# Kernel optimization log

Hardware: AMD Instinct MI355X
Metric: run time of the kernel (lower is better)

## Reference

```python
import jax, jax.numpy as jnp
import numpy as np

B, S, V, D = 4, 2048, 50265, 768
H_LF, DH = 12, 64          # longformer-base heads
C, W = 256, 256            # chunk size, one-sided window
DFF = 3072
NH, DK = 4, 768            # outer MultiHeadAttention(n_head=4, d_k=d_v=768)


def layer_norm(x, g, b, eps=1e-5):
    mu = jnp.mean(x, axis=-1, keepdims=True)
    var = jnp.var(x, axis=-1, keepdims=True)
    return (x - mu) * jax.lax.rsqrt(var + eps) * g + b


def _overlap_chunks(t):
    # t: [B,H,S,dh] -> [B,H,nc,3c,dh] key blocks (chunks j-1,j,j+1, zero-padded at ends)
    nc = S // C
    tp = jnp.pad(t, ((0, 0), (0, 0), (C, C), (0, 0)))
    tr = tp.reshape(t.shape[0], t.shape[1], nc + 2, C, t.shape[-1])
    return jnp.concatenate([tr[:, :, :nc], tr[:, :, 1:nc + 1], tr[:, :, 2:]], axis=3)


def sliding_window_attn(q, k, v):
    # exact band attention: query i attends keys j with |i-j| <= W
    nc = S // C
    qc = q.reshape(q.shape[0], q.shape[1], nc, C, DH)
    kb = _overlap_chunks(k)
    vb = _overlap_chunks(v)
    scores = jnp.einsum('bhncd,bhnkd->bhnck', qc, kb) / np.sqrt(DH)
    ci = jnp.arange(C)[:, None]
    ki = jnp.arange(3 * C)[None, :]
    band = jnp.abs(ki - C - ci) <= W                      # [c,3c]
    n = jnp.arange(nc)[:, None]
    kpos = n * C - C + jnp.arange(3 * C)[None, :]
    valid = (kpos >= 0) & (kpos < S)                      # [nc,3c]
    mask = band[None, :, :] & valid[:, None, :]           # [nc,c,3c]
    scores = jnp.where(mask[None, None], scores, -1e9)
    a = jax.nn.softmax(scores, axis=-1)
    out = jnp.einsum('bhnck,bhnkd->bhncd', a, vb)
    return out.reshape(q.shape)


def longformer_layer(x, emb, pos, ln_e_g, ln_e_b, lf_wq, lf_wk, lf_wv, lf_wo,
                     ln1_g, ln1_b, w1, w2, ln2_g, ln2_b):
    h = layer_norm(emb[x] + pos[None], ln_e_g, ln_e_b)    # [B,S,D]
    def heads(w):
        return (h @ w).reshape(B, S, H_LF, DH).transpose(0, 2, 1, 3)
    q, k, v = heads(lf_wq), heads(lf_wk), heads(lf_wv)
    a = sliding_window_attn(q, k, v)                      # [B,H,S,dh]
    a = a.transpose(0, 2, 1, 3).reshape(B, S, D) @ lf_wo
    h = layer_norm(h + a, ln1_g, ln1_b)
    f = jax.nn.gelu(h @ w1) @ w2
    return layer_norm(h + f, ln2_g, ln2_b)


def mha_and_pool(x, out_lf, mha_wq, mha_wk, mha_wv, mha_fc, mha_ln_g, mha_ln_b):
    residual = out_lf
    def heads(w):
        return (out_lf @ w).reshape(B, S, NH, DK).transpose(0, 2, 1, 3)
    q, k, v = heads(mha_wq), heads(mha_wk), heads(mha_wv)
    scores = jnp.einsum('bhqd,bhkd->bhqk', q, k) / np.sqrt(DK)
    key_mask = (x != 0)[:, None, None, :]
    scores = jnp.where(key_mask, scores, -1e9)
    a = jax.nn.softmax(scores, axis=-1)
    o = jnp.einsum('bhqk,bhkd->bhqd', a, v)
    o = o.transpose(0, 2, 1, 3).reshape(B, S, NH * DK) @ mha_fc
    out_attn = layer_norm(o + residual, mha_ln_g, mha_ln_b)
    return jnp.max(out_attn, axis=1)                      # max_pool1d over seq -> [B,D]


def setup_inputs() -> dict:
    key = jax.random.key(0)
    ks = jax.random.split(key, 16)
    s = 0.02
    d = {
        'x': jax.random.randint(ks[0], (B, S), 0, V),
        'emb': jax.random.normal(ks[1], (V, D), jnp.float32) * s,
        'pos': jax.random.normal(ks[2], (S, D), jnp.float32) * s,
        'ln_e_g': jnp.ones((D,), jnp.float32), 'ln_e_b': jnp.zeros((D,), jnp.float32),
        'lf_wq': jax.random.normal(ks[3], (D, D), jnp.float32) * s,
        'lf_wk': jax.random.normal(ks[4], (D, D), jnp.float32) * s,
        'lf_wv': jax.random.normal(ks[5], (D, D), jnp.float32) * s,
        'lf_wo': jax.random.normal(ks[6], (D, D), jnp.float32) * s,
        'ln1_g': jnp.ones((D,), jnp.float32), 'ln1_b': jnp.zeros((D,), jnp.float32),
        'w1': jax.random.normal(ks[7], (D, DFF), jnp.float32) * s,
        'w2': jax.random.normal(ks[8], (DFF, D), jnp.float32) * s,
        'ln2_g': jnp.ones((D,), jnp.float32), 'ln2_b': jnp.zeros((D,), jnp.float32),
        'mha_wq': jax.random.normal(ks[9], (D, NH * DK), jnp.float32) * s,
        'mha_wk': jax.random.normal(ks[10], (D, NH * DK), jnp.float32) * s,
        'mha_wv': jax.random.normal(ks[11], (D, NH * DK), jnp.float32) * s,
        'mha_fc': jax.random.normal(ks[12], (NH * DK, D), jnp.float32) * s,
        'mha_ln_g': jnp.ones((D,), jnp.float32), 'mha_ln_b': jnp.zeros((D,), jnp.float32),
    }
    return d


def reference(x, emb, pos, ln_e_g, ln_e_b, lf_wq, lf_wk, lf_wv, lf_wo,
              ln1_g, ln1_b, w1, w2, ln2_g, ln2_b,
              mha_wq, mha_wk, mha_wv, mha_fc, mha_ln_g, mha_ln_b):
    out_lf = longformer_layer(x, emb, pos, ln_e_g, ln_e_b, lf_wq, lf_wk, lf_wv, lf_wo,
                              ln1_g, ln1_b, w1, w2, ln2_g, ln2_b)
    out_lf = jax.lax.stop_gradient(out_lf)  # torch.no_grad() around longformer
    return mha_and_pool(x, out_lf, mha_wq, mha_wk, mha_wv, mha_fc, mha_ln_g, mha_ln_b)
```

## Files before the change

### kernel.cpp

```cpp
#include <hip/hip_runtime.h>
#include <hip/hip_bf16.h>
#include <math.h>

#define DEV static __device__ __forceinline__

typedef unsigned short u16;
typedef __attribute__((ext_vector_type(8))) __bf16 bf16x8;
typedef __attribute__((ext_vector_type(4))) float f32x4;

constexpr int SL  = 2048;
constexpr int DM  = 768;
constexpr int CC  = 256;
constexpr int NC  = 8;
constexpr int DH  = 64;
constexpr int DFF = 3072;
constexpr int DKM = 768;

DEV float b2f(u16 u){ union{float f; unsigned u;} c; c.u = ((unsigned)u)<<16; return c.f; }
DEV u16 f2b(float f){ union{float f; unsigned u;} c; c.f=f; unsigned r=(c.u + 0x7fffu + ((c.u>>16)&1u))>>16; return (u16)r; }

DEV void gld16(u16* lds, const u16* g){
  __builtin_amdgcn_global_load_lds((const __attribute__((address_space(1))) void*)g,
                                   (__attribute__((address_space(3))) void*)lds, 16, 0, 0);
}

DEV float wred_sum(float v){
#pragma unroll
  for (int o=32;o;o>>=1) v += __shfl_xor(v,o,64);
  return v;
}
DEV float wred_max(float v){
#pragma unroll
  for (int o=32;o;o>>=1) v = fmaxf(v, __shfl_xor(v,o,64));
  return v;
}
DEV float bred_sum(float v, float* sm){
  v = wred_sum(v);
  if ((threadIdx.x & 63)==0) sm[threadIdx.x>>6] = v;
  __syncthreads();
  float r = sm[0]+sm[1]+sm[2]+sm[3];
  __syncthreads();
  return r;
}
DEV float bred_max(float v, float* sm){
  v = wred_max(v);
  if ((threadIdx.x & 63)==0) sm[threadIdx.x>>6] = v;
  __syncthreads();
  float r = fmaxf(fmaxf(sm[0],sm[1]), fmaxf(sm[2],sm[3]));
  __syncthreads();
  return r;
}

#define MFMA_PH(MH, NH) \
  { _Pragma("unroll") for (int mi2=0; mi2<4; ++mi2) { \
      _Pragma("unroll") for (int ni2=0; ni2<2; ++ni2) { \
        acc[(MH)*4+mi2][(NH)*2+ni2] = __builtin_amdgcn_mfma_f32_16x16x32_bf16(Af[mi2][0], Bf[(NH)*2+ni2][0], acc[(MH)*4+mi2][(NH)*2+ni2], 0,0,0); \
        acc[(MH)*4+mi2][(NH)*2+ni2] = __builtin_amdgcn_mfma_f32_16x16x32_bf16(Af[mi2][1], Bf[(NH)*2+ni2][1], acc[(MH)*4+mi2][(NH)*2+ni2], 0,0,0); } } }

#define PHASE_SYNC \
  __builtin_amdgcn_s_barrier(); \
  asm volatile("s_waitcnt lgkmcnt(0)" ::: "memory"); \
  __builtin_amdgcn_sched_barrier(0); \
  __builtin_amdgcn_s_setprio(1);
#define PHASE_END \
  __builtin_amdgcn_s_setprio(0); \
  __builtin_amdgcn_s_barrier();

template<int MODE, int EPI>
__global__ __launch_bounds__(512,2) void gemm256_k(
    const u16* __restrict__ A, const u16* __restrict__ Bt,
    float* __restrict__ Cf, u16* __restrict__ Cb,
    int K, int lda, int ldb, int ldc)
{
  extern __shared__ u16 lds_dyn[];
  const int tid = threadIdx.x, lane = tid & 63, wv = tid >> 6;
  const int wr = wv >> 2, wc = wv & 3;
  const int m0 = blockIdx.x * 256, n0 = blockIdx.y * 256, z = blockIdx.z;
  const int nt = K >> 6;

  int bb = 0, hh = 0;
  long long baseA = 0, baseB = 0;
  if constexpr (MODE==1) { bb=z>>2; hh=z&3; baseA=(long long)bb*SL*3072 + hh*DKM; baseB=baseA; }
  if constexpr (MODE==2) { bb=z>>2; hh=z&3; baseA=(long long)z*SL*SL; baseB=((long long)bb*3072 + hh*DKM)*SL; }

  const int rb = (wv*64 + lane) >> 3;
  const int sg = ((lane & 7) ^ (rb & 7)) * 8;
  const int rd0 = (lane & 15)*64 + (((lane>>4) ^ (lane & 7)) * 8);
  const int rd1 = rd0 ^ 32;

  auto stageA = [&](int buf, int half, int kt) {
#pragma unroll
    for (int tt = 0; tt < 2; ++tt) {
      const int t = half + tt*2;
      gld16(lds_dyn + buf*16384 + t*4096 + wv*512,
            A + baseA + (long long)(m0 + t*64 + rb)*lda + (long long)kt*64 + sg);
    }
  };
  auto stageB = [&](int buf, int half, int kt) {
#pragma unroll
    for (int tt = 0; tt < 2; ++tt) {
      const int t = half*2 + tt;
      gld16(lds_dyn + 32768 + buf*16384 + t*4096 + wv*512,
            Bt + baseB + (long long)(n0 + t*64 + rb)*ldb + (long long)kt*64 + sg);
    }
  };

  f32x4 acc[8][4] = {};
  bf16x8 Af[4][2];
  bf16x8 Bf[4][2];

  stageA(0,0,0); stageB(0,0,0); stageB(0,1,0); stageA(0,1,0);
  stageA(1,0,1); stageB(1,0,1); stageB(1,1,1);
  asm volatile("s_waitcnt vmcnt(6)" ::: "memory");
  __builtin_amdgcn_s_barrier();

  for (int t = 0; t < nt; ++t) {
    const int d = t & 1;
    const u16* As_d = lds_dyn + d*16384;
    const u16* Bs_d = lds_dyn + 32768 + d*16384;
#pragma unroll
    for (int mi2=0; mi2<4; ++mi2) {
      const u16* p = As_d + (wr*128 + mi2*16)*64;
      Af[mi2][0] = *(const bf16x8*)(p + rd0);
      Af[mi2][1] = *(const bf16x8*)(p + rd1);
    }
#pragma unroll
    for (int ni2=0; ni2<2; ++ni2) {
      const u16* p = Bs_d + (wc*64 + ni2*16)*64;
      Bf[ni2][0] = *(const bf16x8*)(p + rd0);
      Bf[ni2][1] = *(const bf16x8*)(p + rd1);
    }
    if (t+1 < nt) stageA(d^1, 1, t+1);
    PHASE_SYNC; MFMA_PH(0,0); PHASE_END;
#pragma unroll
    for (int ni2=0; ni2<2; ++ni2) {
      const u16* p = Bs_d + (wc*64 + 32 + ni2*16)*64;
      Bf[2+ni2][0] = *(const bf16x8*)(p + rd0);
      Bf[2+ni2][1] = *(const bf16x8*)(p + rd1);
    }
    if (t+2 < nt) stageA(d, 0, t+2);
    PHASE_SYNC; MFMA_PH(0,1); PHASE_END;
#pragma unroll
    for (int mi2=0; mi2<4; ++mi2) {
      const u16* p = As_d + (wr*128 + 64 + mi2*16)*64;
      Af[mi2][0] = *(const bf16x8*)(p + rd0);
      Af[mi2][1] = *(const bf16x8*)(p + rd1);
    }
    if (t+2 < nt) stageB(d, 0, t+2);
    PHASE_SYNC; MFMA_PH(1,0); PHASE_END;
    if (t+2 < nt) stageB(d, 1, t+2);
    __builtin_amdgcn_s_barrier();
    __builtin_amdgcn_s_setprio(1);
    MFMA_PH(1,1);
    __builtin_amdgcn_s_setprio(0);
    if (t+2 < nt)      { asm volatile("s_waitcnt vmcnt(6)" ::: "memory"); }
    else if (t+1 < nt) { asm volatile("s_waitcnt vmcnt(0)" ::: "memory"); }
    __builtin_amdgcn_s_barrier();
  }

#pragma unroll
  for (int mi=0; mi<8; ++mi)
#pragma unroll
  for (int ni=0; ni<4; ++ni)
#pragma unroll
  for (int r=0; r<4; ++r) {
    int m = m0 + wr*128 + mi*16 + ((lane>>4)<<2) + r;
    int n = n0 + wc*64  + ni*16 + (lane & 15);
    float v = acc[mi][ni][r];
    if constexpr (EPI==2) {
      float u = 0.7978845608f*(v + 0.044715f*v*v*v);
      float th = 1.f - 2.f/(__expf(2.f*u)+1.f);
      v = 0.5f*v*(1.f + th);
    }
    if constexpr (EPI==3) v *= 0.0360843918f;
    long long ci;
    if constexpr (MODE==0) ci = (long long)m*ldc + n;
    if constexpr (MODE==1) ci = (long long)z*SL*SL + (long long)m*SL + n;
    if constexpr (MODE==2) ci = ((long long)bb*SL + m)*3072 + hh*DKM + n;
    if constexpr (EPI==0) Cf[ci] = v; else Cb[ci] = f2b(v);
  }
}

template<int BM, int BN, int MODE, int EPI>
__global__ __launch_bounds__(256) void gemm_k(
    const u16* __restrict__ A, const u16* __restrict__ Bt,
    float* __restrict__ Cf, u16* __restrict__ Cb,
    int K, int lda, int ldb, int ldc)
{
  constexpr int BK = 32;
  constexpr int WM = BM/2, WN = BN/2, FM = WM/16, FN = WN/16;
  __shared__ __attribute__((aligned(16))) u16 As[BM*BK];
  __shared__ __attribute__((aligned(16))) u16 Bs[BN*BK];
  const int tid = threadIdx.x, lane = tid & 63, wv = tid >> 6;
  const int wr = wv >> 1, wc = wv & 1;
  const int m0 = blockIdx.x * BM, n0 = blockIdx.y * BN;

  f32x4 acc[FM][FN] = {};

  for (int kt = 0; kt < K; kt += BK) {
#pragma unroll
    for (int t = 0; t < (BM*4)/256; ++t) {
      int cb  = (t*4 + wv)*64;
      int ch  = cb + lane;
      int row = ch >> 2, cp = ch & 3;
      int gp  = cp ^ (row & 3) ^ ((row >> 2) & 1);
      long long ga = (long long)(m0 + row)*lda + (kt + gp*8);
      gld16(&As[cb*8], A + ga);
    }
#pragma unroll
    for (int t = 0; t < (BN*4)/256; ++t) {
      int cb  = (t*4 + wv)*64;
      int ch  = cb + lane;
      int row = ch >> 2, cp = ch & 3;
      int gp  = cp ^ (row & 3) ^ ((row >> 2) & 1);
      long long gb = (long long)(n0 + row)*ldb + (kt + gp*8);
      gld16(&Bs[cb*8], Bt + gb);
    }
    __syncthreads();
    bf16x8 af[FM], bfr[FN];
#pragma unroll
    for (int mi=0; mi<FM; ++mi) {
      int row = wr*WM + mi*16 + (lane & 15);
      int cp  = (lane >> 4) ^ (row & 3) ^ ((row >> 2) & 1);
      af[mi] = *reinterpret_cast<const bf16x8*>(&As[row*BK + cp*8]);
    }
#pragma unroll
    for (int ni=0; ni<FN; ++ni) {
      int row = wc*WN + ni*16 + (lane & 15);
      int cp  = (lane >> 4) ^ (row & 3) ^ ((row >> 2) & 1);
      bfr[ni] = *reinterpret_cast<const bf16x8*>(&Bs[row*BK + cp*8]);
    }
#pragma unroll
    for (int mi=0; mi<FM; ++mi)
#pragma unroll
      for (int ni=0; ni<FN; ++ni)
        acc[mi][ni] = __builtin_amdgcn_mfma_f32_16x16x32_bf16(af[mi], bfr[ni], acc[mi][ni], 0,0,0);
    __syncthreads();
  }

#pragma unroll
  for (int mi=0; mi<FM; ++mi)
#pragma unroll
  for (int ni=0; ni<FN; ++ni)
#pragma unroll
  for (int r=0; r<4; ++r) {
    int m = m0 + wr*WM + mi*16 + ((lane>>4)<<2) + r;
    int n = n0 + wc*WN + ni*16 + (lane & 15);
    float v = acc[mi][ni][r];
    long long ci = (long long)m*ldc + n;
    if constexpr (EPI==0) Cf[ci] = v; else Cb[ci] = f2b(v);
  }
}

__global__ __launch_bounds__(256) void sw_attn_k(
    const u16* __restrict__ Qm, const u16* __restrict__ Km,
    const u16* __restrict__ Vt, u16* __restrict__ Om)
{
  __shared__ __attribute__((aligned(16))) u16 Kb_s[64*64];
  __shared__ __attribute__((aligned(16))) u16 Vb_s[64*64];
  __shared__ __attribute__((aligned(16))) u16 Pb_s[4*32*64];
  const int tid = threadIdx.x, lane = tid & 63, wv = tid >> 6;
  const int qc = blockIdx.x >> 1, half = blockIdx.x & 1;
  const int h = blockIdx.y, b = blockIdx.z;
  const int q0 = qc*256 + half*128 + wv*32;
  const long long rowbase = (long long)b*SL;

  bf16x8 Qf[2][2];
#pragma unroll
  for (int mi=0;mi<2;++mi)
#pragma unroll
    for (int ks=0;ks<2;++ks)
      Qf[mi][ks] = *(const bf16x8*)(Qm + (rowbase + q0 + mi*16 + (lane&15))*DM + h*DH + ks*32 + (lane>>4)*8);

  f32x4 accO[2][4] = {};
  float mrun[2][4], lrun[2][4];
#pragma unroll
  for (int mi=0;mi<2;++mi)
#pragma unroll
    for (int r=0;r<4;++r){ mrun[mi][r]=-3e38f; lrun[mi][r]=0.f; }

  const int srow = tid >> 3;
  const int schunk = (tid & 7) ^ (srow & 7);

  const int kb0 = qc*256 + half*128 - 256;
  const int slo = kb0 < 0 ? ((-kb0) >> 6) : 0;
  const int shi_t = (SL - kb0) >> 6;
  const int shi = shi_t < 10 ? shi_t : 10;

  const int qpb = q0 + ((lane>>4)<<2);

  for (int s = slo; s < shi; ++s) {
    const int kb = kb0 + s*64;
#pragma unroll
    for (int ii=0; ii<2; ++ii) {
      gld16(Kb_s + ii*2048 + wv*512,
            Km + (rowbase + kb + srow + ii*32)*DM + h*DH + schunk*8);
      gld16(Vb_s + ii*2048 + wv*512,
            Vt + ((long long)b*DM + h*DH + srow + ii*32)*SL + kb + schunk*8);
    }
    asm volatile("s_waitcnt vmcnt(0)" ::: "memory");
    __syncthreads();

    f32x4 accS[2][4] = {};
    {
      bf16x8 Kf[4][2];
#pragma unroll
      for (int nf=0;nf<4;++nf){
        int row = nf*16 + (lane&15);
#pragma unroll
        for (int ks=0;ks<2;++ks){
          int ch = ((lane>>4) + ks*4) ^ (row&7);
          Kf[nf][ks] = *(const bf16x8*)(Kb_s + row*64 + ch*8);
        }
      }
#pragma unroll
      for (int mi=0;mi<2;++mi)
#pragma unroll
        for (int nf=0;nf<4;++nf){
          accS[mi][nf] = __builtin_amdgcn_mfma_f32_16x16x32_bf16(Qf[mi][0], Kf[nf][0], accS[mi][nf], 0,0,0);
          accS[mi][nf] = __builtin_amdgcn_mfma_f32_16x16x32_bf16(Qf[mi][1], Kf[nf][1], accS[mi][nf], 0,0,0);
        }
    }

    float smax[2][4];
#pragma unroll
    for (int mi=0;mi<2;++mi)
#pragma unroll
      for (int r=0;r<4;++r) smax[mi][r] = -3e38f;
#pragma unroll
    for (int mi=0;mi<2;++mi)
#pragma unroll
      for (int nf=0;nf<4;++nf)
#pragma unroll
        for (int r=0;r<4;++r){
          int dd = (kb + nf*16 + (lane&15)) - (qpb + mi*16 + r);
          bool ok = (dd <= 256) && (dd >= -256);
          float v = ok ? accS[mi][nf][r]*0.125f : -3e38f;
          accS[mi][nf][r] = v;
          smax[mi][r] = fmaxf(smax[mi][r], v);
        }
#pragma unroll
    for (int mi=0;mi<2;++mi)
#pragma unroll
      for (int r=0;r<4;++r){
        float v = smax[mi][r];
        v = fmaxf(v, __shfl_xor(v,1,64)); v = fmaxf(v, __shfl_xor(v,2,64));
        v = fmaxf(v, __shfl_xor(v,4,64)); v = fmaxf(v, __shfl_xor(v,8,64));
        smax[mi][r] = v;
      }

#pragma unroll
    for (int mi=0;mi<2;++mi)
#pragma unroll
      for (int r=0;r<4;++r){
        float mn = fmaxf(mrun[mi][r], smax[mi][r]);
        float sc = __expf(mrun[mi][r] - mn);
        float ls = 0.f;
#pragma unroll
        for (int nf=0;nf<4;++nf){
          float sv = accS[mi][nf][r];
          float p = (sv > -1e37f) ? __expf(sv - mn) : 0.f;
          accS[mi][nf][r] = p;
          ls += p;
        }
        ls += __shfl_xor(ls,1,64); ls += __shfl_xor(ls,2,64);
        ls += __shfl_xor(ls,4,64); ls += __shfl_xor(ls,8,64);
        lrun[mi][r] = lrun[mi][r]*sc + ls;
        mrun[mi][r] = mn;
#pragma unroll
        for (int df=0;df<4;++df) accO[mi][df][r] *= sc;
      }
#pragma unroll
    for (int mi=0;mi<2;++mi)
#pragma unroll
      for (int nf=0;nf<4;++nf)
#pragma unroll
        for (int r=0;r<4;++r){
          int ql = mi*16 + ((lane>>4)<<2) + r;
          int k  = nf*16 + (lane&15);
          int ch = (k>>3) ^ (ql&7);
          Pb_s[wv*2048 + ql*64 + ch*8 + (k&7)] = f2b(accS[mi][nf][r]);
        }
    asm volatile("s_waitcnt lgkmcnt(0)" ::: "memory");
    __builtin_amdgcn_sched_barrier(0);

    {
      bf16x8 Pf[2][2], Vf[4][2];
#pragma unroll
      for (int mi=0;mi<2;++mi){
        int ql = mi*16 + (lane&15);
#pragma unroll
        for (int ks=0;ks<2;++ks){
          int ch = ((lane>>4) + ks*4) ^ (ql&7);
          Pf[mi][ks] = *(const bf16x8*)(Pb_s + wv*2048 + ql*64 + ch*8);
        }
      }
#pragma unroll
      for (int df=0;df<4;++df){
        int dr = df*16 + (lane&15);
#pragma unroll
        for (int ks=0;ks<2;++ks){
          int ch = ((lane>>4) + ks*4) ^ (dr&7);
          Vf[df][ks] = *(const bf16x8*)(Vb_s + dr*64 + ch*8);
        }
      }
#pragma unroll
      for (int mi=0;mi<2;++mi)
#pragma unroll
        for (int df=0;df<4;++df){
          accO[mi][df] = __builtin_amdgcn_mfma_f32_16x16x32_bf16(Pf[mi][0], Vf[df][0], accO[mi][df], 0,0,0);
          accO[mi][df] = __builtin_amdgcn_mfma_f32_16x16x32_bf16(Pf[mi][1], Vf[df][1], accO[mi][df], 0,0,0);
        }
    }
    __syncthreads();
  }

#pragma unroll
  for (int mi=0;mi<2;++mi)
#pragma unroll
    for (int df=0;df<4;++df)
#pragma unroll
      for (int r=0;r<4;++r){
        long long row = rowbase + qpb + mi*16 + r;
        int col = h*DH + df*16 + (lane&15);
        Om[row*DM + col] = f2b(accO[mi][df][r] / lrun[mi][r]);
      }
}

__global__ __launch_bounds__(256) void embed_ln_k(const int* __restrict__ x,
    const float* __restrict__ emb, const float* __restrict__ pos,
    const float* __restrict__ g, const float* __restrict__ bta,
    float* __restrict__ of, u16* __restrict__ ob)
{
  __shared__ float sm[4];
  const int row = blockIdx.x, s = row & (SL-1);
  const long long tok = x[row];
  const float* e = emb + tok*DM;
  const float* p = pos + (long long)s*DM;
  float v[3], su=0.f, sq=0.f;
#pragma unroll
  for (int i=0;i<3;++i){ int d=threadIdx.x+i*256; v[i]=e[d]+p[d]; su+=v[i]; sq+=v[i]*v[i]; }
  su = bred_sum(su, sm); sq = bred_sum(sq, sm);
  float mean = su*(1.f/DM), var = sq*(1.f/DM)-mean*mean, rs = rsqrtf(var+1e-5f);
#pragma unroll
  for (int i=0;i<3;++i){ int d=threadIdx.x+i*256;
    float o = (v[i]-mean)*rs*g[d] + bta[d];
    of[(long long)row*DM+d]=o; ob[(long long)row*DM+d]=f2b(o); }
}

__global__ __launch_bounds__(256) void resid_ln_k(const float* __restrict__ a, const float* __restrict__ c,
    const float* __restrict__ g, const float* __restrict__ bta,
    float* __restrict__ of, u16* __restrict__ ob)
{
  __shared__ float sm[4];
  const long long row = blockIdx.x;
  const float* ra = a + row*DM;
  const float* rc = c + row*DM;
  float v[3], su=0.f, sq=0.f;
#pragma unroll
  for (int i=0;i<3;++i){ int d=threadIdx.x+i*256; v[i]=ra[d]+rc[d]; su+=v[i]; sq+=v[i]*v[i]; }
  su = bred_sum(su, sm); sq = bred_sum(sq, sm);
  float mean = su*(1.f/DM), var = sq*(1.f/DM)-mean*mean, rs = rsqrtf(var+1e-5f);
#pragma unroll
  for (int i=0;i<3;++i){ int d=threadIdx.x+i*256;
    float o = (v[i]-mean)*rs*g[d] + bta[d];
    of[row*DM+d]=o; if (ob) ob[row*DM+d]=f2b(o); }
}

__global__ __launch_bounds__(256) void transp_w_k(const float* __restrict__ W, u16* __restrict__ Wt, int Kd, int Nd)
{
  __shared__ float t[32][33];
  int n0 = blockIdx.x*32, k0 = blockIdx.y*32;
  int lx = threadIdx.x & 31, ly = threadIdx.x >> 5;
#pragma unroll
  for (int i=0;i<4;++i) t[ly+i*8][lx] = W[(long long)(k0+ly+i*8)*Nd + n0+lx];
  __syncthreads();
#pragma unroll
  for (int i=0;i<4;++i) Wt[(long long)(n0+ly+i*8)*Kd + k0+lx] = f2b(t[lx][ly+i*8]);
}

__global__ __launch_bounds__(256) void transp_b_k(const u16* __restrict__ in, u16* __restrict__ out, int Nc)
{
  __shared__ u16 t[32][33];
  int c0 = blockIdx.x*32, r0 = blockIdx.y*32;
  int lx = threadIdx.x & 31, ly = threadIdx.x >> 5;
#pragma unroll
  for (int i=0;i<4;++i) t[ly+i*8][lx] = in[(long long)(r0+ly+i*8)*Nc + c0+lx];
  __syncthreads();
  int b = r0 >> 11, s0 = r0 & (SL-1);
#pragma unroll
  for (int i=0;i<4;++i) out[((long long)b*Nc + c0+ly+i*8)*SL + s0+lx] = t[lx][ly+i*8];
}

__global__ __launch_bounds__(256) void mha_softmax_k(u16* __restrict__ sc, const int* __restrict__ x)
{
  __shared__ float sm[4];
  const int rid = blockIdx.x;
  const int qi = rid & (SL-1);
  const int z  = rid >> 11;
  const int b  = z >> 2;
  u16* row = sc + (long long)z*SL*SL + (long long)qi*SL;
  const int* xb = x + b*SL;
  float v[8]; float mx = -3e38f;
#pragma unroll
  for (int i=0;i<8;++i){
    int j = threadIdx.x + i*256;
    bool ok = xb[j] != 0;
    v[i] = ok ? b2f(row[j]) : -3e38f;
    mx = fmaxf(mx, v[i]);
  }
  mx = bred_max(mx, sm);
  float s = 0.f;
#pragma unroll
  for (int i=0;i<8;++i){ v[i] = (v[i] > -1e37f) ? __expf(v[i]-mx) : 0.f; s += v[i]; }
  s = bred_sum(s, sm);
  float inv = 1.f/s;
#pragma unroll
  for (int i=0;i<8;++i){ int j = threadIdx.x + i*256; row[j] = f2b(v[i]*inv); }
}

__global__ __launch_bounds__(256) void pool_part_k(const float* __restrict__ f, float* __restrict__ pp)
{
  int b = blockIdx.x, ch = blockIdx.y;
  float m0=-3e38f, m1=-3e38f, m2=-3e38f;
  for (int s = ch*128; s < ch*128+128; ++s){
    const float* r = f + ((long long)b*SL + s)*DM;
    m0=fmaxf(m0,r[threadIdx.x]); m1=fmaxf(m1,r[threadIdx.x+256]); m2=fmaxf(m2,r[threadIdx.x+512]);
  }
  float* o = pp + (long long)(b*16+ch)*DM;
  o[threadIdx.x]=m0; o[threadIdx.x+256]=m1; o[threadIdx.x+512]=m2;
}

__global__ __launch_bounds__(256) void pool_red_k(const float* __restrict__ pp, float* __restrict__ out)
{
  int b = blockIdx.x;
#pragma unroll
  for (int i=0;i<3;++i){
    int d = threadIdx.x + i*256;
    float m = -3e38f;
    for (int c=0;c<16;++c) m = fmaxf(m, pp[(long long)(b*16+c)*DM + d]);
    out[(long long)b*DM + d] = m;
  }
}

extern "C" void kernel_launch(void* const* d_in, const int* in_sizes, int n_in,
                              void* d_out, int out_size, void* d_ws, size_t ws_size,
                              hipStream_t stream)
{
  const int*   x      = (const int*)  d_in[0];
  const float* emb    = (const float*)d_in[1];
  const float* pos    = (const float*)d_in[2];
  const float* ln_e_g = (const float*)d_in[3];
  const float* ln_e_b = (const float*)d_in[4];
  const float* lf_wq  = (const float*)d_in[5];
  const float* lf_wk  = (const float*)d_in[6];
  const float* lf_wv  = (const float*)d_in[7];
  const float* lf_wo  = (const float*)d_in[8];
  const float* ln1_g  = (const float*)d_in[9];
  const float* ln1_b  = (const float*)d_in[10];
  const float* w1     = (const float*)d_in[11];
  const float* w2     = (const float*)d_in[12];
  const float* ln2_g  = (const float*)d_in[13];
  const float* ln2_b  = (const float*)d_in[14];
  const float* mha_wq = (const float*)d_in[15];
  const float* mha_wk = (const float*)d_in[16];
  const float* mha_wv = (const float*)d_in[17];
  const float* mha_fc = (const float*)d_in[18];
  const float* mha_ln_g = (const float*)d_in[19];
  const float* mha_ln_b = (const float*)d_in[20];

  (void)hipFuncSetAttribute((const void*)gemm256_k<0,1>, hipFuncAttributeMaxDynamicSharedMemorySize, 131072);
  (void)hipFuncSetAttribute((const void*)gemm256_k<0,2>, hipFuncAttributeMaxDynamicSharedMemorySize, 131072);
  (void)hipFuncSetAttribute((const void*)gemm256_k<1,3>, hipFuncAttributeMaxDynamicSharedMemorySize, 131072);
  (void)hipFuncSetAttribute((const void*)gemm256_k<2,1>, hipFuncAttributeMaxDynamicSharedMemorySize, 131072);

  const long long R = 8192;
  float* F0 = (float*)d_ws;
  float* F1 = F0 + R*DM;
  float* F2 = F1 + R*DM;
  u16* B0 = (u16*)(F2 + R*DM);
  u16* B1 = B0 + R*DM;
  u16* B2 = B1 + R*DM;
  u16* B3 = B2 + R*DM;
  u16* WT = B3 + R*DM;
  u16* G1 = WT + (long long)DFF*DM;
  u16* G2 = G1 + R*DFF;
  u16* G3 = G2 + R*DFF;
  u16* SC = G3 + R*DFF;
  float* PP = (float*)(SC + (long long)4*12*NC*CC*768);

  dim3 T(256), T5(512);
  const size_t SMEM = 131072;
  embed_ln_k<<<dim3(8192), T, 0, stream>>>(x, emb, pos, ln_e_g, ln_e_b, F0, B0);

  transp_w_k<<<dim3(24,24), T, 0, stream>>>(lf_wq, WT, DM, DM);
  gemm_k<128,128,0,1><<<dim3(64,6), T, 0, stream>>>(B0, WT, nullptr, B1, DM, DM, DM, DM);
  transp_w_k<<<dim3(24,24), T, 0, stream>>>(lf_wk, WT, DM, DM);
  gemm_k<128,128,0,1><<<dim3(64,6), T, 0, stream>>>(B0, WT, nullptr, B2, DM, DM, DM, DM);
  transp_w_k<<<dim3(24,24), T, 0, stream>>>(lf_wv, WT, DM, DM);
  gemm_k<128,128,0,1><<<dim3(64,6), T, 0, stream>>>(B0, WT, nullptr, SC, DM, DM, DM, DM);
  transp_b_k<<<dim3(24,256), T, 0, stream>>>(SC, B3, DM);

  sw_attn_k<<<dim3(16,12,4), T, 0, stream>>>(B1, B2, B3, B0);

  transp_w_k<<<dim3(24,24), T, 0, stream>>>(lf_wo, WT, DM, DM);
  gemm_k<128,128,0,0><<<dim3(64,6), T, 0, stream>>>(B0, WT, F1, nullptr, DM, DM, DM, DM);
  resid_ln_k<<<dim3(8192), T, 0, stream>>>(F0, F1, ln1_g, ln1_b, F2, B1);

  transp_w_k<<<dim3(96,24), T, 0, stream>>>(w1, WT, DM, DFF);
  gemm256_k<0,2><<<dim3(32,12,1), T5, SMEM, stream>>>(B1, WT, nullptr, G1, DM, DM, DM, DFF);
  transp_w_k<<<dim3(24,96), T, 0, stream>>>(w2, WT, DFF, DM);
  gemm_k<128,128,0,0><<<dim3(64,6), T, 0, stream>>>(G1, WT, F1, nullptr, DFF, DFF, DFF, DM);
  resid_ln_k<<<dim3(8192), T, 0, stream>>>(F2, F1, ln2_g, ln2_b, F0, B2);

  transp_w_k<<<dim3(96,24), T, 0, stream>>>(mha_wq, WT, DM, DFF);
  gemm256_k<0,1><<<dim3(32,12,1), T5, SMEM, stream>>>(B2, WT, nullptr, G1, DM, DM, DM, DFF);
  transp_w_k<<<dim3(96,24), T, 0, stream>>>(mha_wk, WT, DM, DFF);
  gemm256_k<0,1><<<dim3(32,12,1), T5, SMEM, stream>>>(B2, WT, nullptr, G2, DM, DM, DM, DFF);
  transp_w_k<<<dim3(96,24), T, 0, stream>>>(mha_wv, WT, DM, DFF);
  gemm256_k<0,1><<<dim3(32,12,1), T5, SMEM, stream>>>(B2, WT, nullptr, SC, DM, DM, DM, DFF);
  transp_b_k<<<dim3(96,256), T, 0, stream>>>(SC, G3, DFF);

  gemm256_k<1,3><<<dim3(8,8,16), T5, SMEM, stream>>>(G1, G2, nullptr, SC, DKM, 3072, 3072, 0);
  mha_softmax_k<<<dim3(32768), T, 0, stream>>>(SC, x);
  gemm256_k<2,1><<<dim3(8,3,16), T5, SMEM, stream>>>(SC, G3, nullptr, G1, SL, SL, SL, 0);

  transp_w_k<<<dim3(24,96), T, 0, stream>>>(mha_fc, WT, DFF, DM);
  gemm_k<128,128,0,0><<<dim3(64,6), T, 0, stream>>>(G1, WT, F1, nullptr, DFF, DFF, DFF, DM);
  resid_ln_k<<<dim3(8192), T, 0, stream>>>(F0, F1, mha_ln_g, mha_ln_b, F2, nullptr);

  pool_part_k<<<dim3(4,16), T, 0, stream>>>(F2, PP);
  pool_red_k<<<dim3(4), T, 0, stream>>>(PP, (float*)d_out);
}
```

Measured before the change: 1.040 ms.

## Fuse QKV projections, add 256x128 PV GEMM, vectorize MHA softmax

The Longformer Q/K/V projections and the outer MHA Q/K/V projections are each merged into a single GEMM launch over concatenated transposed weights, with the epilogue routing columns to three output buffers. The attention-times-V GEMM moves to a new 256x128-tile kernel that launches a larger grid for better CU fill, and its output goes to G2 so the Q buffer is not overwritten. The MHA softmax now processes one row per wavefront with 16-byte vector loads and wave-only reductions, dropping the block-level syncs. The cost is a larger weight workspace plus a per-element segment branch in the GEMM epilogue.

```diff
diff --git a/kernel.cpp b/kernel.cpp
--- a/kernel.cpp
+++ b/kernel.cpp
@@ -6,12 +6,13 @@
 
 typedef unsigned short u16;
 typedef __attribute__((ext_vector_type(8))) __bf16 bf16x8;
+typedef __attribute__((ext_vector_type(8))) unsigned short u16x8;
 typedef __attribute__((ext_vector_type(4))) float f32x4;
+typedef __attribute__((ext_vector_type(4))) int i32x4;
 
 constexpr int SL  = 2048;
 constexpr int DM  = 768;
 constexpr int CC  = 256;
-constexpr int NC  = 8;
 constexpr int DH  = 64;
 constexpr int DFF = 3072;
 constexpr int DKM = 768;
@@ -42,20 +43,6 @@
   __syncthreads();
   return r;
 }
-DEV float bred_max(float v, float* sm){
-  v = wred_max(v);
-  if ((threadIdx.x & 63)==0) sm[threadIdx.x>>6] = v;
-  __syncthreads();
-  float r = fmaxf(fmaxf(sm[0],sm[1]), fmaxf(sm[2],sm[3]));
-  __syncthreads();
-  return r;
-}
-
-#define MFMA_PH(MH, NH) \
-  { _Pragma("unroll") for (int mi2=0; mi2<4; ++mi2) { \
-      _Pragma("unroll") for (int ni2=0; ni2<2; ++ni2) { \
-        acc[(MH)*4+mi2][(NH)*2+ni2] = __builtin_amdgcn_mfma_f32_16x16x32_bf16(Af[mi2][0], Bf[(NH)*2+ni2][0], acc[(MH)*4+mi2][(NH)*2+ni2], 0,0,0); \
-        acc[(MH)*4+mi2][(NH)*2+ni2] = __builtin_amdgcn_mfma_f32_16x16x32_bf16(Af[mi2][1], Bf[(NH)*2+ni2][1], acc[(MH)*4+mi2][(NH)*2+ni2], 0,0,0); } } }
 
 #define PHASE_SYNC \
   __builtin_amdgcn_s_barrier(); \
@@ -66,10 +53,17 @@
   __builtin_amdgcn_s_setprio(0); \
   __builtin_amdgcn_s_barrier();
 
+#define MFMA_PH(MH, NH) \
+  { _Pragma("unroll") for (int mi2=0; mi2<4; ++mi2) { \
+      _Pragma("unroll") for (int ni2=0; ni2<2; ++ni2) { \
+        acc[(MH)*4+mi2][(NH)*2+ni2] = __builtin_amdgcn_mfma_f32_16x16x32_bf16(Af[mi2][0], Bf[(NH)*2+ni2][0], acc[(MH)*4+mi2][(NH)*2+ni2], 0,0,0); \
+        acc[(MH)*4+mi2][(NH)*2+ni2] = __builtin_amdgcn_mfma_f32_16x16x32_bf16(Af[mi2][1], Bf[(NH)*2+ni2][1], acc[(MH)*4+mi2][(NH)*2+ni2], 0,0,0); } } }
+
 template<int MODE, int EPI>
 __global__ __launch_bounds__(512,2) void gemm256_k(
     const u16* __restrict__ A, const u16* __restrict__ Bt,
     float* __restrict__ Cf, u16* __restrict__ Cb,
+    u16* __restrict__ Cb2, u16* __restrict__ Cb3,
     int K, int lda, int ldb, int ldc)
 {
   extern __shared__ u16 lds_dyn[];
@@ -81,7 +75,6 @@
   int bb = 0, hh = 0;
   long long baseA = 0, baseB = 0;
   if constexpr (MODE==1) { bb=z>>2; hh=z&3; baseA=(long long)bb*SL*3072 + hh*DKM; baseB=baseA; }
-  if constexpr (MODE==2) { bb=z>>2; hh=z&3; baseA=(long long)z*SL*SL; baseB=((long long)bb*3072 + hh*DKM)*SL; }
 
   const int rb = (wv*64 + lane) >> 3;
   const int sg = ((lane & 7) ^ (rb & 7)) * 8;
@@ -173,11 +166,117 @@
       v = 0.5f*v*(1.f + th);
     }
     if constexpr (EPI==3) v *= 0.0360843918f;
-    long long ci;
-    if constexpr (MODE==0) ci = (long long)m*ldc + n;
-    if constexpr (MODE==1) ci = (long long)z*SL*SL + (long long)m*SL + n;
-    if constexpr (MODE==2) ci = ((long long)bb*SL + m)*3072 + hh*DKM + n;
-    if constexpr (EPI==0) Cf[ci] = v; else Cb[ci] = f2b(v);
+    if constexpr (MODE==3) {
+      int seg = n / 3072, nn = n - seg*3072;
+      u16* dst = seg==0 ? Cb : (seg==1 ? Cb2 : Cb3);
+      dst[(long long)m*3072 + nn] = f2b(v);
+    } else {
+      long long ci;
+      if constexpr (MODE==1) ci = (long long)z*SL*SL + (long long)m*SL + n;
+      else                   ci = (long long)m*ldc + n;
+      if constexpr (EPI==0) Cf[ci] = v; else Cb[ci] = f2b(v);
+    }
+  }
+}
+
+#define MFMA_Q(MB, NB, AF) \
+  { _Pragma("unroll") for (int mi2=0; mi2<2; ++mi2) { \
+      _Pragma("unroll") for (int ni2=0; ni2<2; ++ni2) { \
+        acc[(MB)+mi2][(NB)+ni2] = __builtin_amdgcn_mfma_f32_16x16x32_bf16(AF[mi2][0], Bf[(NB)+ni2][0], acc[(MB)+mi2][(NB)+ni2], 0,0,0); \
+        acc[(MB)+mi2][(NB)+ni2] = __builtin_amdgcn_mfma_f32_16x16x32_bf16(AF[mi2][1], Bf[(NB)+ni2][1], acc[(MB)+mi2][(NB)+ni2], 0,0,0); } } }
+
+__global__ __launch_bounds__(512,2) void gemm128n_k(
+    const u16* __restrict__ A, const u16* __restrict__ Bt, u16* __restrict__ Cb, int K)
+{
+  extern __shared__ u16 lds_dyn[];
+  const int tid = threadIdx.x, lane = tid & 63, wv = tid >> 6;
+  const int wr = wv >> 1, wc = wv & 1;
+  const int m0 = blockIdx.x * 256, n0 = blockIdx.y * 128, z = blockIdx.z;
+  const int bb = z >> 2, hh = z & 3;
+  const long long baseA = (long long)z*SL*SL;
+  const long long baseB = ((long long)bb*3072 + hh*DKM)*SL;
+  const int nt = K >> 6;
+
+  const int rb = (wv*64 + lane) >> 3;
+  const int sg = ((lane & 7) ^ (rb & 7)) * 8;
+  const int rd0 = (lane & 15)*64 + (((lane>>4) ^ (lane & 7)) * 8);
+  const int rd1 = rd0 ^ 32;
+
+  auto stageA = [&](int buf, int half, int kt) {
+#pragma unroll
+    for (int tt = 0; tt < 2; ++tt) {
+      const int t = half*2 + tt;
+      gld16(lds_dyn + buf*16384 + t*4096 + wv*512,
+            A + baseA + (long long)(m0 + t*64 + rb)*SL + (long long)kt*64 + sg);
+    }
+  };
+  auto stageB = [&](int buf, int idx, int kt) {
+    gld16(lds_dyn + 32768 + buf*8192 + idx*4096 + wv*512,
+          Bt + baseB + (long long)(n0 + idx*64 + rb)*SL + (long long)kt*64 + sg);
+  };
+
+  f32x4 acc[4][4] = {};
+  bf16x8 Af[2][2];
+  bf16x8 Bf[4][2];
+
+  stageA(0,0,0); stageB(0,0,0); stageB(0,1,0); stageA(0,1,0);
+  stageA(1,0,1); stageB(1,0,1); stageB(1,1,1);
+  asm volatile("s_waitcnt vmcnt(4)" ::: "memory");
+  __builtin_amdgcn_s_barrier();
+
+  for (int t = 0; t < nt; ++t) {
+    const int d = t & 1;
+    const u16* As_d = lds_dyn + d*16384;
+    const u16* Bs_d = lds_dyn + 32768 + d*8192;
+#pragma unroll
+    for (int mi2=0; mi2<2; ++mi2) {
+      const u16* p = As_d + (wr*32 + mi2*16)*64;
+      Af[mi2][0] = *(const bf16x8*)(p + rd0);
+      Af[mi2][1] = *(const bf16x8*)(p + rd1);
+    }
+#pragma unroll
+    for (int ni2=0; ni2<2; ++ni2) {
+      const u16* p = Bs_d + (wc*64 + ni2*16)*64;
+      Bf[ni2][0] = *(const bf16x8*)(p + rd0);
+      Bf[ni2][1] = *(const bf16x8*)(p + rd1);
+    }
+    if (t+1 < nt) stageA(d^1, 1, t+1);
+    PHASE_SYNC; MFMA_Q(0,0,Af); PHASE_END;
+#pragma unroll
+    for (int ni2=0; ni2<2; ++ni2) {
+      const u16* p = Bs_d + (wc*64 + 32 + ni2*16)*64;
+      Bf[2+ni2][0] = *(const bf16x8*)(p + rd0);
+      Bf[2+ni2][1] = *(const bf16x8*)(p + rd1);
+    }
+    if (t+2 < nt) stageA(d, 0, t+2);
+    PHASE_SYNC; MFMA_Q(0,2,Af); PHASE_END;
+#pragma unroll
+    for (int mi2=0; mi2<2; ++mi2) {
+      const u16* p = As_d + (128 + wr*32 + mi2*16)*64;
+      Af[mi2][0] = *(const bf16x8*)(p + rd0);
+      Af[mi2][1] = *(const bf16x8*)(p + rd1);
+    }
+    if (t+2 < nt) stageB(d, 0, t+2);
+    PHASE_SYNC; MFMA_Q(2,0,Af); PHASE_END;
+    if (t+2 < nt) stageB(d, 1, t+2);
+    __builtin_amdgcn_s_barrier();
+    __builtin_amdgcn_s_setprio(1);
+    MFMA_Q(2,2,Af);
+    __builtin_amdgcn_s_setprio(0);
+    if (t+2 < nt)      { asm volatile("s_waitcnt vmcnt(4)" ::: "memory"); }
+    else if (t+1 < nt) { asm volatile("s_waitcnt vmcnt(0)" ::: "memory"); }
+    __builtin_amdgcn_s_barrier();
+  }
+
+#pragma unroll
+  for (int mi=0; mi<4; ++mi)
+#pragma unroll
+  for (int ni=0; ni<4; ++ni)
+#pragma unroll
+  for (int r=0; r<4; ++r) {
+    int m = m0 + (mi>>1)*128 + wr*32 + (mi&1)*16 + ((lane>>4)<<2) + r;
+    int n = n0 + wc*64 + ni*16 + (lane & 15);
+    Cb[((long long)bb*SL + m)*3072 + hh*DKM + n] = f2b(acc[mi][ni][r]);
   }
 }
 
@@ -185,6 +284,7 @@
 __global__ __launch_bounds__(256) void gemm_k(
     const u16* __restrict__ A, const u16* __restrict__ Bt,
     float* __restrict__ Cf, u16* __restrict__ Cb,
+    u16* __restrict__ Cb2, u16* __restrict__ Cb3,
     int K, int lda, int ldb, int ldc)
 {
   constexpr int BK = 32;
@@ -247,8 +347,14 @@
     int m = m0 + wr*WM + mi*16 + ((lane>>4)<<2) + r;
     int n = n0 + wc*WN + ni*16 + (lane & 15);
     float v = acc[mi][ni][r];
-    long long ci = (long long)m*ldc + n;
-    if constexpr (EPI==0) Cf[ci] = v; else Cb[ci] = f2b(v);
+    if constexpr (MODE==5) {
+      int seg = n / 768, nn = n - seg*768;
+      u16* dst = seg==0 ? Cb : (seg==1 ? Cb2 : Cb3);
+      dst[(long long)m*768 + nn] = f2b(v);
+    } else {
+      long long ci = (long long)m*ldc + n;
+      if constexpr (EPI==0) Cf[ci] = v; else Cb[ci] = f2b(v);
+    }
   }
 }
 
@@ -494,29 +600,40 @@
 
 __global__ __launch_bounds__(256) void mha_softmax_k(u16* __restrict__ sc, const int* __restrict__ x)
 {
-  __shared__ float sm[4];
-  const int rid = blockIdx.x;
-  const int qi = rid & (SL-1);
-  const int z  = rid >> 11;
-  const int b  = z >> 2;
-  u16* row = sc + (long long)z*SL*SL + (long long)qi*SL;
+  const int r = blockIdx.x*4 + (threadIdx.x >> 6);
+  const int lane = threadIdx.x & 63;
+  const int z = r >> 11;
+  const int b = z >> 2;
+  u16* row = sc + (long long)z*SL*SL + (long long)(r & (SL-1))*SL;
   const int* xb = x + b*SL;
-  float v[8]; float mx = -3e38f;
-#pragma unroll
-  for (int i=0;i<8;++i){
-    int j = threadIdx.x + i*256;
-    bool ok = xb[j] != 0;
-    v[i] = ok ? b2f(row[j]) : -3e38f;
-    mx = fmaxf(mx, v[i]);
-  }
-  mx = bred_max(mx, sm);
+  float v[32]; float mx = -3e38f;
+#pragma unroll
+  for (int i=0;i<4;++i){
+    const int j0 = i*512 + lane*8;
+    u16x8 pv = *(const u16x8*)(row + j0);
+    i32x4 xa = *(const i32x4*)(xb + j0);
+    i32x4 xc = *(const i32x4*)(xb + j0 + 4);
+#pragma unroll
+    for (int e=0;e<8;++e){
+      int xv = e<4 ? xa[e] : xc[e-4];
+      float f = (xv != 0) ? b2f(pv[e]) : -3e38f;
+      v[i*8+e] = f;
+      mx = fmaxf(mx, f);
+    }
+  }
+  mx = wred_max(mx);
   float s = 0.f;
 #pragma unroll
-  for (int i=0;i<8;++i){ v[i] = (v[i] > -1e37f) ? __expf(v[i]-mx) : 0.f; s += v[i]; }
-  s = bred_sum(s, sm);
+  for (int i=0;i<32;++i){ v[i] = (v[i] > -1e37f) ? __expf(v[i]-mx) : 0.f; s += v[i]; }
+  s = wred_sum(s);
   float inv = 1.f/s;
 #pragma unroll
-  for (int i=0;i<8;++i){ int j = threadIdx.x + i*256; row[j] = f2b(v[i]*inv); }
+  for (int i=0;i<4;++i){
+    u16x8 ov;
+#pragma unroll
+    for (int e=0;e<8;++e) ov[e] = f2b(v[i*8+e]*inv);
+    *(u16x8*)(row + i*512 + lane*8) = ov;
+  }
 }
 
 __global__ __launch_bounds__(256) void pool_part_k(const float* __restrict__ f, float* __restrict__ pp)
@@ -569,10 +686,10 @@
   const float* mha_ln_g = (const float*)d_in[19];
   const float* mha_ln_b = (const float*)d_in[20];
 
-  (void)hipFuncSetAttribute((const void*)gemm256_k<0,1>, hipFuncAttributeMaxDynamicSharedMemorySize, 131072);
   (void)hipFuncSetAttribute((const void*)gemm256_k<0,2>, hipFuncAttributeMaxDynamicSharedMemorySize, 131072);
   (void)hipFuncSetAttribute((const void*)gemm256_k<1,3>, hipFuncAttributeMaxDynamicSharedMemorySize, 131072);
-  (void)hipFuncSetAttribute((const void*)gemm256_k<2,1>, hipFuncAttributeMaxDynamicSharedMemorySize, 131072);
+  (void)hipFuncSetAttribute((const void*)gemm256_k<3,1>, hipFuncAttributeMaxDynamicSharedMemorySize, 131072);
+  (void)hipFuncSetAttribute((const void*)gemm128n_k,     hipFuncAttributeMaxDynamicSharedMemorySize, 98304);
 
   const long long R = 8192;
   float* F0 = (float*)d_ws;
@@ -583,50 +700,47 @@
   u16* B2 = B1 + R*DM;
   u16* B3 = B2 + R*DM;
   u16* WT = B3 + R*DM;
-  u16* G1 = WT + (long long)DFF*DM;
+  u16* G1 = WT + (long long)9216*DM;
   u16* G2 = G1 + R*DFF;
   u16* G3 = G2 + R*DFF;
   u16* SC = G3 + R*DFF;
-  float* PP = (float*)(SC + (long long)4*12*NC*CC*768);
+  float* PP = (float*)(SC + (long long)16*SL*SL);
 
   dim3 T(256), T5(512);
-  const size_t SMEM = 131072;
+  const size_t SM256 = 131072, SM128 = 98304;
+
   embed_ln_k<<<dim3(8192), T, 0, stream>>>(x, emb, pos, ln_e_g, ln_e_b, F0, B0);
 
-  transp_w_k<<<dim3(24,24), T, 0, stream>>>(lf_wq, WT, DM, DM);
-  gemm_k<128,128,0,1><<<dim3(64,6), T, 0, stream>>>(B0, WT, nullptr, B1, DM, DM, DM, DM);
-  transp_w_k<<<dim3(24,24), T, 0, stream>>>(lf_wk, WT, DM, DM);
-  gemm_k<128,128,0,1><<<dim3(64,6), T, 0, stream>>>(B0, WT, nullptr, B2, DM, DM, DM, DM);
-  transp_w_k<<<dim3(24,24), T, 0, stream>>>(lf_wv, WT, DM, DM);
-  gemm_k<128,128,0,1><<<dim3(64,6), T, 0, stream>>>(B0, WT, nullptr, SC, DM, DM, DM, DM);
+  transp_w_k<<<dim3(24,24), T, 0, stream>>>(lf_wq, WT,               DM, DM);
+  transp_w_k<<<dim3(24,24), T, 0, stream>>>(lf_wk, WT + 768*768,     DM, DM);
+  transp_w_k<<<dim3(24,24), T, 0, stream>>>(lf_wv, WT + 2*768*768,   DM, DM);
+  gemm_k<128,128,5,1><<<dim3(64,18), T, 0, stream>>>(B0, WT, nullptr, B1, B2, SC, DM, DM, DM, 0);
   transp_b_k<<<dim3(24,256), T, 0, stream>>>(SC, B3, DM);
 
   sw_attn_k<<<dim3(16,12,4), T, 0, stream>>>(B1, B2, B3, B0);
 
   transp_w_k<<<dim3(24,24), T, 0, stream>>>(lf_wo, WT, DM, DM);
-  gemm_k<128,128,0,0><<<dim3(64,6), T, 0, stream>>>(B0, WT, F1, nullptr, DM, DM, DM, DM);
+  gemm_k<128,128,0,0><<<dim3(64,6), T, 0, stream>>>(B0, WT, F1, nullptr, nullptr, nullptr, DM, DM, DM, DM);
   resid_ln_k<<<dim3(8192), T, 0, stream>>>(F0, F1, ln1_g, ln1_b, F2, B1);
 
   transp_w_k<<<dim3(96,24), T, 0, stream>>>(w1, WT, DM, DFF);
-  gemm256_k<0,2><<<dim3(32,12,1), T5, SMEM, stream>>>(B1, WT, nullptr, G1, DM, DM, DM, DFF);
+  gemm256_k<0,2><<<dim3(32,12,1), T5, SM256, stream>>>(B1, WT, nullptr, G1, nullptr, nullptr, DM, DM, DM, DFF);
   transp_w_k<<<dim3(24,96), T, 0, stream>>>(w2, WT, DFF, DM);
-  gemm_k<128,128,0,0><<<dim3(64,6), T, 0, stream>>>(G1, WT, F1, nullptr, DFF, DFF, DFF, DM);
+  gemm_k<128,128,0,0><<<dim3(64,6), T, 0, stream>>>(G1, WT, F1, nullptr, nullptr, nullptr, DFF, DFF, DFF, DM);
   resid_ln_k<<<dim3(8192), T, 0, stream>>>(F2, F1, ln2_g, ln2_b, F0, B2);
 
-  transp_w_k<<<dim3(96,24), T, 0, stream>>>(mha_wq, WT, DM, DFF);
-  gemm256_k<0,1><<<dim3(32,12,1), T5, SMEM, stream>>>(B2, WT, nullptr, G1, DM, DM, DM, DFF);
-  transp_w_k<<<dim3(96,24), T, 0, stream>>>(mha_wk, WT, DM, DFF);
-  gemm256_k<0,1><<<dim3(32,12,1), T5, SMEM, stream>>>(B2, WT, nullptr, G2, DM, DM, DM, DFF);
-  transp_w_k<<<dim3(96,24), T, 0, stream>>>(mha_wv, WT, DM, DFF);
-  gemm256_k<0,1><<<dim3(32,12,1), T5, SMEM, stream>>>(B2, WT, nullptr, SC, DM, DM, DM, DFF);
+  transp_w_k<<<dim3(96,24), T, 0, stream>>>(mha_wq, WT,                 DM, DFF);
+  transp_w_k<<<dim3(96,24), T, 0, stream>>>(mha_wk, WT + (long long)3072*768, DM, DFF);
+  transp_w_k<<<dim3(96,24), T, 0, stream>>>(mha_wv, WT + (long long)6144*768, DM, DFF);
+  gemm256_k<3,1><<<dim3(32,36,1), T5, SM256, stream>>>(B2, WT, nullptr, G1, G2, SC, DM, DM, DM, 0);
   transp_b_k<<<dim3(96,256), T, 0, stream>>>(SC, G3, DFF);
 
-  gemm256_k<1,3><<<dim3(8,8,16), T5, SMEM, stream>>>(G1, G2, nullptr, SC, DKM, 3072, 3072, 0);
-  mha_softmax_k<<<dim3(32768), T, 0, stream>>>(SC, x);
-  gemm256_k<2,1><<<dim3(8,3,16), T5, SMEM, stream>>>(SC, G3, nullptr, G1, SL, SL, SL, 0);
+  gemm256_k<1,3><<<dim3(8,8,16), T5, SM256, stream>>>(G1, G2, nullptr, SC, nullptr, nullptr, DKM, 3072, 3072, 0);
+  mha_softmax_k<<<dim3(8192), T, 0, stream>>>(SC, x);
+  gemm128n_k<<<dim3(8,6,16), T5, SM128, stream>>>(SC, G3, G2, SL);
 
   transp_w_k<<<dim3(24,96), T, 0, stream>>>(mha_fc, WT, DFF, DM);
-  gemm_k<128,128,0,0><<<dim3(64,6), T, 0, stream>>>(G1, WT, F1, nullptr, DFF, DFF, DFF, DM);
+  gemm_k<128,128,0,0><<<dim3(64,6), T, 0, stream>>>(G2, WT, F1, nullptr, nullptr, nullptr, DFF, DFF, DFF, DM);
   resid_ln_k<<<dim3(8192), T, 0, stream>>>(F0, F1, mha_ln_g, mha_ln_b, F2, nullptr);
 
   pool_part_k<<<dim3(4,16), T, 0, stream>>>(F2, PP);
```

After: 926.6 us. -10.9%, faster.
